# Optimization experiments

Hardware: AMD Instinct MI355X
Metric: run time of the kernel (lower is better)

The kernel has to match this reference:

```python
import jax, jax.numpy as jnp
import numpy as np

B, C, H, W = 4, 256, 64, 64
CR = max(C // 8, 1)  # reduced channels
EPS = 1e-12  # F.normalize eps


def setup_inputs() -> dict:
    key = jax.random.key(0)
    ks = jax.random.split(key, 8)
    s = 1.0 / np.sqrt(C)
    return {
        "x": jax.random.normal(ks[0], (B, C, H, W), dtype=jnp.float32),
        "Wq": jax.random.normal(ks[1], (CR, C), dtype=jnp.float32) * s,
        "bq": jax.random.normal(ks[2], (CR,), dtype=jnp.float32) * s,
        "Wk": jax.random.normal(ks[3], (CR, C), dtype=jnp.float32) * s,
        "bk": jax.random.normal(ks[4], (CR,), dtype=jnp.float32) * s,
        "Wv": jax.random.normal(ks[5], (C, C), dtype=jnp.float32) * s,
        "bv": jax.random.normal(ks[6], (C,), dtype=jnp.float32) * s,
        "gamma": jax.random.normal(ks[7], (1,), dtype=jnp.float32),
    }


def reference(x, Wq, bq, Wk, bk, Wv, bv, gamma):
    b, c, h, w = x.shape
    xf = x.reshape(b, c, h * w)  # [B, C, N]
    # 1x1 convs are per-pixel linear maps
    q = jnp.einsum("rc,bcn->brn", Wq, xf) + bq[None, :, None]  # [B, CR, N]
    k = jnp.einsum("rc,bcn->brn", Wk, xf) + bk[None, :, None]  # [B, CR, N]
    v = jnp.einsum("dc,bcn->bdn", Wv, xf) + bv[None, :, None]  # [B, C, N]
    # attention = bmm(key^T, query): [B, N, N]
    attn = jnp.einsum("brn,brm->bnm", k, q)
    attn = jax.nn.relu(attn)
    # L1 normalize along dim=1 (rows), matching F.normalize(p=1, dim=1)
    denom = jnp.maximum(jnp.sum(jnp.abs(attn), axis=1, keepdims=True), EPS)
    attn = attn / denom
    out = jnp.einsum("bcn,bnm->bcm", v, attn).reshape(b, c, h, w)
    return gamma[0] * out + x
```

## Files before the change

### kernel.cpp

```cpp
#include <hip/hip_runtime.h>
#include <hip/hip_bf16.h>

#define NB 4
#define NC 256
#define NN 4096
#define NCR 32

typedef __attribute__((ext_vector_type(8))) short short8_t;
typedef __attribute__((ext_vector_type(4))) float f32x4;
typedef __attribute__((ext_vector_type(2))) int int2_t;
typedef __attribute__((ext_vector_type(4))) int int4_t;
typedef __attribute__((ext_vector_type(4))) float float4_t;

static __device__ __forceinline__ unsigned short f2bf(float f) {
  unsigned u = __builtin_bit_cast(unsigned, f);
  u += 0x7FFFu + ((u >> 16) & 1u);
  return (unsigned short)(u >> 16);
}

static __device__ __forceinline__ unsigned cvt_pk(float lo, float hi) {
  unsigned r;
  asm("v_cvt_pk_bf16_f32 %0, %1, %2" : "=v"(r) : "v"(lo), "v"(hi));
  return r;
}

__global__ __launch_bounds__(64) void pack_w_kernel(
    const float* __restrict__ Wq, const float* __restrict__ Wk,
    const float* __restrict__ Wv, unsigned short* __restrict__ Wbf)
{
  const int row = blockIdx.x;
  const int t = threadIdx.x;
  const float* src = row < 32 ? Wq + (size_t)row * NC
                   : (row < 64 ? Wk + (size_t)(row - 32) * NC
                               : Wv + (size_t)(row - 64) * NC);
  float4_t v = *(const float4_t*)(src + t * 4);
  int2_t p;
  p[0] = cvt_pk(v[0], v[1]);
  p[1] = cvt_pk(v[2], v[3]);
  *(int2_t*)(Wbf + (size_t)row * NC + t * 4) = p;
}

__global__ __launch_bounds__(256) void qkv_kernel(
    const float* __restrict__ x, const unsigned short* __restrict__ Wbf,
    const float* __restrict__ bq, const float* __restrict__ bk,
    const float* __restrict__ bv,
    unsigned short* __restrict__ Qt, unsigned short* __restrict__ Kt,
    unsigned short* __restrict__ Vt)
{
  __shared__ unsigned short xT[2][64 * 32];

  const int bid = blockIdx.x;
  const int b   = bid >> 6;
  const int m0  = (bid & 63) * 64;
  const int tid = threadIdx.x;
  const int w    = tid >> 6;
  const int lane = tid & 63;
  const int lg   = lane >> 4;
  const int lm   = lane & 15;

  const float* xb = x + (size_t)b * NC * NN;
  const float* xld = xb + (size_t)(8 * w) * NN + m0 + lane;
  const int wofs = lane * 32 + ((w ^ (lane & 3)) << 3);
  const unsigned short* wrow = Wbf + (size_t)(w * 80 + lm) * NC;

  const f32x4 zero4 = {0.f, 0.f, 0.f, 0.f};
  f32x4 acc[5][4];
#pragma unroll
  for (int df = 0; df < 5; df++)
#pragma unroll
    for (int mf = 0; mf < 4; mf++) acc[df][mf] = zero4;

  float xg[8], xn[8];
#pragma unroll
  for (int j = 0; j < 8; j++) xg[j] = xld[j * NN];

#define QSTEP(KC, XC, XN, BUF) {                                              \
    if ((KC) < 7) {                                                           \
      _Pragma("unroll") for (int j = 0; j < 8; j++)                           \
        XN[j] = xld[(((KC) + 1) * 32 + j) * NN];                              \
    }                                                                         \
    short8_t wf[5];                                                           \
    _Pragma("unroll") for (int df = 0; df < 5; df++)                          \
      wf[df] = *(const short8_t*)(wrow + df * 16 * NC + (KC) * 32 + lg * 8);  \
    int4_t xw;                                                                \
    xw[0] = cvt_pk(XC[0], XC[1]); xw[1] = cvt_pk(XC[2], XC[3]);               \
    xw[2] = cvt_pk(XC[4], XC[5]); xw[3] = cvt_pk(XC[6], XC[7]);               \
    *(int4_t*)(&xT[BUF][wofs]) = xw;                                          \
    __syncthreads();                                                          \
    short8_t xf[4];                                                           \
    _Pragma("unroll") for (int mf = 0; mf < 4; mf++)                          \
      xf[mf] = *(const short8_t*)(&xT[BUF][(mf * 16 + lm) * 32 +              \
                                          ((lg ^ (lm & 3)) << 3)]);           \
    _Pragma("unroll") for (int df = 0; df < 5; df++)                          \
      _Pragma("unroll") for (int mf = 0; mf < 4; mf++)                        \
        acc[df][mf] = __builtin_amdgcn_mfma_f32_16x16x32_bf16(                \
            xf[mf], wf[df], acc[df][mf], 0, 0, 0);                            \
  }

#pragma unroll
  for (int kc = 0; kc < 8; kc += 2) {
    QSTEP(kc, xg, xn, 0)
    QSTEP(kc + 1, xn, xg, 1)
  }
#undef QSTEP

#pragma unroll
  for (int df = 0; df < 5; df++) {
    const int dbase = w * 80 + df * 16;
    if (dbase < 64) {
      const bool isq = dbase < 32;
      const float bia = isq ? bq[dbase + lm] : bk[dbase - 32 + lm];
      unsigned short* dst = isq ? Qt : Kt;
      const int dcol = (isq ? dbase : dbase - 32) + lm;
#pragma unroll
      for (int mf = 0; mf < 4; mf++)
#pragma unroll
        for (int i = 0; i < 4; i++) {
          const int m = m0 + mf * 16 + lg * 4 + i;
          dst[((size_t)b * NN + m) * NCR + dcol] = f2bf(acc[df][mf][i] + bia);
        }
    } else {
      const int c = dbase - 64 + lm;
      const float bia = bv[c];
#pragma unroll
      for (int mf = 0; mf < 4; mf++) {
        int2_t p;
        p[0] = cvt_pk(acc[df][mf][0] + bia, acc[df][mf][1] + bia);
        p[1] = cvt_pk(acc[df][mf][2] + bia, acc[df][mf][3] + bia);
        *(int2_t*)(Vt + ((size_t)b * NC + c) * NN + m0 + mf * 16 + lg * 4) = p;
      }
    }
  }
}

__global__ __launch_bounds__(256) void attn_kernel(
    const unsigned short* __restrict__ Qt, const unsigned short* __restrict__ Kt,
    const unsigned short* __restrict__ Vt, const float* __restrict__ x,
    const float* __restrict__ gamma, float* __restrict__ out)
{
  __shared__ unsigned short Slds[2][64 * 72];
  __shared__ float dlds[4][64];

  int bid = blockIdx.x;
  bid = (bid & 7) * 32 + (bid >> 3);
  const int b   = bid >> 6;
  const int m0  = (bid & 63) * 64;
  const int tid = threadIdx.x;
  const int w    = tid >> 6;
  const int lane = tid & 63;
  const int lg   = lane >> 4;
  const int lm   = lane & 15;

  const unsigned short* Qb = Qt + (size_t)b * NN * NCR;
  const unsigned short* Kb = Kt + (size_t)b * NN * NCR + (w * 16 + lm) * NCR + lg * 8;
  const unsigned short* Vb = Vt + (size_t)b * NC * NN;
  const unsigned short* pV[4];
#pragma unroll
  for (int cf = 0; cf < 4; cf++)
    pV[cf] = Vb + (size_t)(w * 64 + cf * 16 + lm) * NN + lg * 8;

  short8_t qf[4];
#pragma unroll
  for (int mf = 0; mf < 4; mf++)
    qf[mf] = *(const short8_t*)(Qb + (size_t)(m0 + mf * 16 + lm) * NCR + lg * 8);

  const f32x4 zero4 = {0.f, 0.f, 0.f, 0.f};
  f32x4 acc[4][4];
#pragma unroll
  for (int cf = 0; cf < 4; cf++)
#pragma unroll
    for (int mf = 0; mf < 4; mf++) acc[cf][mf] = zero4;
  float dsum[4] = {0.f, 0.f, 0.f, 0.f};

  short8_t kA, kB, vA[4][2], vB[4][2];
  kA = *(const short8_t*)(Kb);
#pragma unroll
  for (int cf = 0; cf < 4; cf++)
#pragma unroll
    for (int nch = 0; nch < 2; nch++)
      vA[cf][nch] = *(const short8_t*)(pV[cf] + nch * 32);

  const int swofs = w * 16 + lg * 4;

#define AITER(T, VC, VN, KC, KN, BUF) {                                       \
    const int n1 = (((T) + 1) & 63) * 64;                                     \
    KN = *(const short8_t*)(Kb + (size_t)n1 * NCR);                           \
    _Pragma("unroll") for (int cf = 0; cf < 4; cf++)                          \
      _Pragma("unroll") for (int nch = 0; nch < 2; nch++)                     \
        VN[cf][nch] = *(const short8_t*)(pV[cf] + n1 + nch * 32);             \
    _Pragma("unroll") for (int mf = 0; mf < 4; mf++) {                        \
      f32x4 s = __builtin_amdgcn_mfma_f32_16x16x32_bf16(KC, qf[mf], zero4, 0, 0, 0); \
      float s0 = fmaxf(s[0], 0.f), s1 = fmaxf(s[1], 0.f);                     \
      float s2 = fmaxf(s[2], 0.f), s3 = fmaxf(s[3], 0.f);                     \
      dsum[mf] += (s0 + s1) + (s2 + s3);                                      \
      int2_t p; p[0] = cvt_pk(s0, s1); p[1] = cvt_pk(s2, s3);                 \
      *(int2_t*)(&Slds[BUF][(mf * 16 + lm) * 72 + swofs]) = p;                \
    }                                                                         \
    __syncthreads();                                                          \
    _Pragma("unroll") for (int nch = 0; nch < 2; nch++) {                     \
      short8_t sf[4];                                                         \
      _Pragma("unroll") for (int mf = 0; mf < 4; mf++)                        \
        sf[mf] = *(const short8_t*)(&Slds[BUF][(mf * 16 + lm) * 72 + nch * 32 + lg * 8]); \
      _Pragma("unroll") for (int cf = 0; cf < 4; cf++)                        \
        _Pragma("unroll") for (int mf = 0; mf < 4; mf++)                      \
          acc[cf][mf] = __builtin_amdgcn_mfma_f32_16x16x32_bf16(              \
              VC[cf][nch], sf[mf], acc[cf][mf], 0, 0, 0);                     \
    }                                                                         \
  }

#pragma unroll 1
  for (int t = 0; t < 64; t += 2) {
    AITER(t, vA, vB, kA, kB, 0)
    AITER(t + 1, vB, vA, kB, kA, 1)
  }
#undef AITER

#pragma unroll
  for (int mf = 0; mf < 4; mf++) {
    float v = dsum[mf];
    v += __shfl_xor(v, 16);
    v += __shfl_xor(v, 32);
    dsum[mf] = v;
  }
  if (lane < 16) {
#pragma unroll
    for (int mf = 0; mf < 4; mf++) dlds[w][mf * 16 + lane] = dsum[mf];
  }
  __syncthreads();

  const float g0 = gamma[0];
  float rden[4];
#pragma unroll
  for (int mf = 0; mf < 4; mf++) {
    const int mloc = mf * 16 + lm;
    float den = dlds[0][mloc] + dlds[1][mloc] + dlds[2][mloc] + dlds[3][mloc];
    den = den > 1e-12f ? den : 1e-12f;
    rden[mf] = 1.0f / den;
  }

  const float* xb = x + (size_t)b * NC * NN;
  float* ob = out + (size_t)b * NC * NN;
#pragma unroll
  for (int cf = 0; cf < 4; cf++) {
#pragma unroll
    for (int i = 0; i < 4; i++) {
      const int c = w * 64 + cf * 16 + lg * 4 + i;
#pragma unroll
      for (int mf = 0; mf < 4; mf++) {
        const int m = m0 + mf * 16 + lm;
        ob[(size_t)c * NN + m] = g0 * acc[cf][mf][i] * rden[mf] + xb[(size_t)c * NN + m];
      }
    }
  }
}

extern "C" void kernel_launch(void* const* d_in, const int* in_sizes, int n_in,
                              void* d_out, int out_size, void* d_ws, size_t ws_size,
                              hipStream_t stream) {
  const float* x     = (const float*)d_in[0];
  const float* Wq    = (const float*)d_in[1];
  const float* bq    = (const float*)d_in[2];
  const float* Wk    = (const float*)d_in[3];
  const float* bk    = (const float*)d_in[4];
  const float* Wv    = (const float*)d_in[5];
  const float* bv    = (const float*)d_in[6];
  const float* gamma = (const float*)d_in[7];
  float* out = (float*)d_out;

  unsigned short* Wbf = (unsigned short*)d_ws;
  unsigned short* Qt  = Wbf + (size_t)320 * NC;
  unsigned short* Kt  = Qt + (size_t)NB * NN * NCR;
  unsigned short* Vt  = Kt + (size_t)NB * NN * NCR;

  hipLaunchKernelGGL(pack_w_kernel, dim3(320), dim3(64), 0, stream,
                     Wq, Wk, Wv, Wbf);
  hipLaunchKernelGGL(qkv_kernel, dim3(256), dim3(256), 0, stream,
                     x, Wbf, bq, bk, bv, Qt, Kt, Vt);
  hipLaunchKernelGGL(attn_kernel, dim3(256), dim3(256), 0, stream,
                     Qt, Kt, Vt, x, gamma, out);
}
```

Measured before the change: 88.24 us.

## Split attention channels across blocks and precompute bf16 transposed input

Adds a kernel that transposes x to a bf16 [B,N,C] layout, so qkv_kernel reads MFMA fragments straight from global memory with no LDS staging, using 32-pixel tiles and twice as many blocks. The attention kernel now splits the 256 output channels into two halves across blocks, giving 512 blocks with 2 waves' worth of occupancy. It also maps batch and half to XCD id, drops V double-buffering in favour of in-iteration loads, and raises wave priority around the MFMA section. The cost is recomputing the QK scores twice (once per channel half), an extra kernel launch, and a round trip for the transposed x buffer.

```diff
diff --git a/kernel.cpp b/kernel.cpp
--- a/kernel.cpp
+++ b/kernel.cpp
@@ -5,6 +5,7 @@
 #define NC 256
 #define NN 4096
 #define NCR 32
+#define PITCH 72
 
 typedef __attribute__((ext_vector_type(8))) short short8_t;
 typedef __attribute__((ext_vector_type(4))) float f32x4;
@@ -40,69 +41,69 @@
   *(int2_t*)(Wbf + (size_t)row * NC + t * 4) = p;
 }
 
-__global__ __launch_bounds__(256) void qkv_kernel(
-    const float* __restrict__ x, const unsigned short* __restrict__ Wbf,
+__global__ __launch_bounds__(256) void xpose_kernel(
+    const float* __restrict__ x, unsigned short* __restrict__ xT)
+{
+  __shared__ float tile[32][65];
+  const int bid = blockIdx.x;
+  const int mt = bid & 63, kt = (bid >> 6) & 7, b = bid >> 9;
+  const int m0 = mt * 64, k0 = kt * 32;
+  const int tid = threadIdx.x;
+
+  const float* xb = x + (size_t)b * NC * NN + (size_t)k0 * NN + m0;
+#pragma unroll
+  for (int p = 0; p < 8; p++) {
+    const int r = p * 4 + (tid >> 6);
+    tile[r][tid & 63] = xb[(size_t)r * NN + (tid & 63)];
+  }
+  __syncthreads();
+
+  const int m = tid >> 2, kq = (tid & 3) * 8;
+  int4_t o;
+#pragma unroll
+  for (int j = 0; j < 4; j++)
+    o[j] = cvt_pk(tile[kq + 2 * j][m], tile[kq + 2 * j + 1][m]);
+  *(int4_t*)(xT + ((size_t)b * NN + m0 + m) * NC + k0 + kq) = o;
+}
+
+__global__ __launch_bounds__(256, 2) void qkv_kernel(
+    const unsigned short* __restrict__ xT, const unsigned short* __restrict__ Wbf,
     const float* __restrict__ bq, const float* __restrict__ bk,
     const float* __restrict__ bv,
     unsigned short* __restrict__ Qt, unsigned short* __restrict__ Kt,
     unsigned short* __restrict__ Vt)
 {
-  __shared__ unsigned short xT[2][64 * 32];
-
   const int bid = blockIdx.x;
-  const int b   = bid >> 6;
-  const int m0  = (bid & 63) * 64;
+  const int b   = bid >> 7;
+  const int m0  = (bid & 127) * 32;
   const int tid = threadIdx.x;
   const int w    = tid >> 6;
   const int lane = tid & 63;
   const int lg   = lane >> 4;
   const int lm   = lane & 15;
 
-  const float* xb = x + (size_t)b * NC * NN;
-  const float* xld = xb + (size_t)(8 * w) * NN + m0 + lane;
-  const int wofs = lane * 32 + ((w ^ (lane & 3)) << 3);
-  const unsigned short* wrow = Wbf + (size_t)(w * 80 + lm) * NC;
+  const unsigned short* xrow0 = xT + ((size_t)b * NN + m0 + lm) * NC + lg * 8;
+  const unsigned short* xrow1 = xrow0 + 16 * NC;
+  const unsigned short* wrow  = Wbf + (size_t)(w * 80 + lm) * NC + lg * 8;
 
   const f32x4 zero4 = {0.f, 0.f, 0.f, 0.f};
-  f32x4 acc[5][4];
+  f32x4 acc[5][2];
 #pragma unroll
   for (int df = 0; df < 5; df++)
 #pragma unroll
-    for (int mf = 0; mf < 4; mf++) acc[df][mf] = zero4;
-
-  float xg[8], xn[8];
-#pragma unroll
-  for (int j = 0; j < 8; j++) xg[j] = xld[j * NN];
-
-#define QSTEP(KC, XC, XN, BUF) {                                              \
-    if ((KC) < 7) {                                                           \
-      _Pragma("unroll") for (int j = 0; j < 8; j++)                           \
-        XN[j] = xld[(((KC) + 1) * 32 + j) * NN];                              \
-    }                                                                         \
-    short8_t wf[5];                                                           \
-    _Pragma("unroll") for (int df = 0; df < 5; df++)                          \
-      wf[df] = *(const short8_t*)(wrow + df * 16 * NC + (KC) * 32 + lg * 8);  \
-    int4_t xw;                                                                \
-    xw[0] = cvt_pk(XC[0], XC[1]); xw[1] = cvt_pk(XC[2], XC[3]);               \
-    xw[2] = cvt_pk(XC[4], XC[5]); xw[3] = cvt_pk(XC[6], XC[7]);               \
-    *(int4_t*)(&xT[BUF][wofs]) = xw;                                          \
-    __syncthreads();                                                          \
-    short8_t xf[4];                                                           \
-    _Pragma("unroll") for (int mf = 0; mf < 4; mf++)                          \
-      xf[mf] = *(const short8_t*)(&xT[BUF][(mf * 16 + lm) * 32 +              \
-                                          ((lg ^ (lm & 3)) << 3)]);           \
-    _Pragma("unroll") for (int df = 0; df < 5; df++)                          \
-      _Pragma("unroll") for (int mf = 0; mf < 4; mf++)                        \
-        acc[df][mf] = __builtin_amdgcn_mfma_f32_16x16x32_bf16(                \
-            xf[mf], wf[df], acc[df][mf], 0, 0, 0);                            \
-  }
-
-#pragma unroll
-  for (int kc = 0; kc < 8; kc += 2) {
-    QSTEP(kc, xg, xn, 0)
-    QSTEP(kc + 1, xn, xg, 1)
-  }
-#undef QSTEP
+    for (int mf = 0; mf < 2; mf++) acc[df][mf] = zero4;
+
+#pragma unroll
+  for (int kc = 0; kc < 8; kc++) {
+    const short8_t xf0 = *(const short8_t*)(xrow0 + kc * 32);
+    const short8_t xf1 = *(const short8_t*)(xrow1 + kc * 32);
+#pragma unroll
+    for (int df = 0; df < 5; df++) {
+      const short8_t wf = *(const short8_t*)(wrow + (size_t)df * 16 * NC + kc * 32);
+      acc[df][0] = __builtin_amdgcn_mfma_f32_16x16x32_bf16(xf0, wf, acc[df][0], 0, 0, 0);
+      acc[df][1] = __builtin_amdgcn_mfma_f32_16x16x32_bf16(xf1, wf, acc[df][1], 0, 0, 0);
+    }
+  }
 
 #pragma unroll
   for (int df = 0; df < 5; df++) {
@@ -113,7 +114,7 @@
       unsigned short* dst = isq ? Qt : Kt;
       const int dcol = (isq ? dbase : dbase - 32) + lm;
 #pragma unroll
-      for (int mf = 0; mf < 4; mf++)
+      for (int mf = 0; mf < 2; mf++)
 #pragma unroll
         for (int i = 0; i < 4; i++) {
           const int m = m0 + mf * 16 + lg * 4 + i;
@@ -123,7 +124,7 @@
       const int c = dbase - 64 + lm;
       const float bia = bv[c];
 #pragma unroll
-      for (int mf = 0; mf < 4; mf++) {
+      for (int mf = 0; mf < 2; mf++) {
         int2_t p;
         p[0] = cvt_pk(acc[df][mf][0] + bia, acc[df][mf][1] + bia);
         p[1] = cvt_pk(acc[df][mf][2] + bia, acc[df][mf][3] + bia);
@@ -133,18 +134,19 @@
   }
 }
 
-__global__ __launch_bounds__(256) void attn_kernel(
+__global__ __launch_bounds__(256, 2) void attn_kernel(
     const unsigned short* __restrict__ Qt, const unsigned short* __restrict__ Kt,
     const unsigned short* __restrict__ Vt, const float* __restrict__ x,
     const float* __restrict__ gamma, float* __restrict__ out)
 {
-  __shared__ unsigned short Slds[2][64 * 72];
+  __shared__ unsigned short Slds[2][64 * PITCH];
   __shared__ float dlds[4][64];
 
-  int bid = blockIdx.x;
-  bid = (bid & 7) * 32 + (bid >> 3);
-  const int b   = bid >> 6;
-  const int m0  = (bid & 63) * 64;
+  const int bid = blockIdx.x;
+  const int xcd = bid & 7;
+  const int b   = xcd >> 1;
+  const int ch  = xcd & 1;
+  const int m0  = (bid >> 3) * 64;
   const int tid = threadIdx.x;
   const int w    = tid >> 6;
   const int lane = tid & 63;
@@ -152,12 +154,12 @@
   const int lm   = lane & 15;
 
   const unsigned short* Qb = Qt + (size_t)b * NN * NCR;
-  const unsigned short* Kb = Kt + (size_t)b * NN * NCR + (w * 16 + lm) * NCR + lg * 8;
-  const unsigned short* Vb = Vt + (size_t)b * NC * NN;
-  const unsigned short* pV[4];
-#pragma unroll
-  for (int cf = 0; cf < 4; cf++)
-    pV[cf] = Vb + (size_t)(w * 64 + cf * 16 + lm) * NN + lg * 8;
+  const unsigned short* Kp = Kt + (size_t)b * NN * NCR +
+                             (size_t)(w * 16 + lm) * NCR + lg * 8;
+  const unsigned short* pV[2];
+#pragma unroll
+  for (int cf = 0; cf < 2; cf++)
+    pV[cf] = Vt + ((size_t)b * NC + ch * 128 + w * 32 + cf * 16 + lm) * NN + lg * 8;
 
   short8_t qf[4];
 #pragma unroll
@@ -165,53 +167,55 @@
     qf[mf] = *(const short8_t*)(Qb + (size_t)(m0 + mf * 16 + lm) * NCR + lg * 8);
 
   const f32x4 zero4 = {0.f, 0.f, 0.f, 0.f};
-  f32x4 acc[4][4];
-#pragma unroll
-  for (int cf = 0; cf < 4; cf++)
+  f32x4 acc[2][4];
+#pragma unroll
+  for (int cf = 0; cf < 2; cf++)
 #pragma unroll
     for (int mf = 0; mf < 4; mf++) acc[cf][mf] = zero4;
   float dsum[4] = {0.f, 0.f, 0.f, 0.f};
 
-  short8_t kA, kB, vA[4][2], vB[4][2];
-  kA = *(const short8_t*)(Kb);
-#pragma unroll
-  for (int cf = 0; cf < 4; cf++)
-#pragma unroll
-    for (int nch = 0; nch < 2; nch++)
-      vA[cf][nch] = *(const short8_t*)(pV[cf] + nch * 32);
+  short8_t kA, kB;
+  kA = *(const short8_t*)(Kp);
 
   const int swofs = w * 16 + lg * 4;
 
-#define AITER(T, VC, VN, KC, KN, BUF) {                                       \
+#define AITER(T, KC, KN, BUF) {                                               \
+    const int ncur = (T) * 64;                                                \
+       \
+    short8_t vc[2][2];                                                        \
+    _Pragma("unroll") for (int cf = 0; cf < 2; cf++) {                        \
+      vc[cf][0] = *(const short8_t*)(pV[cf] + ncur);                          \
+      vc[cf][1] = *(const short8_t*)(pV[cf] + ncur + 32);                     \
+    }                                                                         \
     const int n1 = (((T) + 1) & 63) * 64;                                     \
-    KN = *(const short8_t*)(Kb + (size_t)n1 * NCR);                           \
-    _Pragma("unroll") for (int cf = 0; cf < 4; cf++)                          \
-      _Pragma("unroll") for (int nch = 0; nch < 2; nch++)                     \
-        VN[cf][nch] = *(const short8_t*)(pV[cf] + n1 + nch * 32);             \
+    KN = *(const short8_t*)(Kp + (size_t)n1 * NCR);                           \
     _Pragma("unroll") for (int mf = 0; mf < 4; mf++) {                        \
       f32x4 s = __builtin_amdgcn_mfma_f32_16x16x32_bf16(KC, qf[mf], zero4, 0, 0, 0); \
       float s0 = fmaxf(s[0], 0.f), s1 = fmaxf(s[1], 0.f);                     \
       float s2 = fmaxf(s[2], 0.f), s3 = fmaxf(s[3], 0.f);                     \
       dsum[mf] += (s0 + s1) + (s2 + s3);                                      \
       int2_t p; p[0] = cvt_pk(s0, s1); p[1] = cvt_pk(s2, s3);                 \
-      *(int2_t*)(&Slds[BUF][(mf * 16 + lm) * 72 + swofs]) = p;                \
+      *(int2_t*)(&Slds[BUF][(mf * 16 + lm) * PITCH + swofs]) = p;             \
     }                                                                         \
     __syncthreads();                                                          \
+    __builtin_amdgcn_s_setprio(1);                                            \
     _Pragma("unroll") for (int nch = 0; nch < 2; nch++) {                     \
       short8_t sf[4];                                                         \
       _Pragma("unroll") for (int mf = 0; mf < 4; mf++)                        \
-        sf[mf] = *(const short8_t*)(&Slds[BUF][(mf * 16 + lm) * 72 + nch * 32 + lg * 8]); \
-      _Pragma("unroll") for (int cf = 0; cf < 4; cf++)                        \
+        sf[mf] = *(const short8_t*)(&Slds[BUF][(mf * 16 + lm) * PITCH +       \
+                                              nch * 32 + lg * 8]);            \
+      _Pragma("unroll") for (int cf = 0; cf < 2; cf++)                        \
         _Pragma("unroll") for (int mf = 0; mf < 4; mf++)                      \
           acc[cf][mf] = __builtin_amdgcn_mfma_f32_16x16x32_bf16(              \
-              VC[cf][nch], sf[mf], acc[cf][mf], 0, 0, 0);                     \
+              vc[cf][nch], sf[mf], acc[cf][mf], 0, 0, 0);                     \
     }                                                                         \
+    __builtin_amdgcn_s_setprio(0);                                            \
   }
 
 #pragma unroll 1
   for (int t = 0; t < 64; t += 2) {
-    AITER(t, vA, vB, kA, kB, 0)
-    AITER(t + 1, vB, vA, kB, kA, 1)
+    AITER(t, kA, kB, 0)
+    AITER(t + 1, kB, kA, 1)
   }
 #undef AITER
 
@@ -220,11 +224,7 @@
     float v = dsum[mf];
     v += __shfl_xor(v, 16);
     v += __shfl_xor(v, 32);
-    dsum[mf] = v;
-  }
-  if (lane < 16) {
-#pragma unroll
-    for (int mf = 0; mf < 4; mf++) dlds[w][mf * 16 + lane] = dsum[mf];
+    if (lane < 16) dlds[w][mf * 16 + lane] = v;
   }
   __syncthreads();
 
@@ -241,10 +241,10 @@
   const float* xb = x + (size_t)b * NC * NN;
   float* ob = out + (size_t)b * NC * NN;
 #pragma unroll
-  for (int cf = 0; cf < 4; cf++) {
+  for (int cf = 0; cf < 2; cf++) {
 #pragma unroll
     for (int i = 0; i < 4; i++) {
-      const int c = w * 64 + cf * 16 + lg * 4 + i;
+      const int c = ch * 128 + w * 32 + cf * 16 + lg * 4 + i;
 #pragma unroll
       for (int mf = 0; mf < 4; mf++) {
         const int m = m0 + mf * 16 + lm;
@@ -268,14 +268,16 @@
   float* out = (float*)d_out;
 
   unsigned short* Wbf = (unsigned short*)d_ws;
-  unsigned short* Qt  = Wbf + (size_t)320 * NC;
+  unsigned short* xT  = Wbf + (size_t)320 * NC;
+  unsigned short* Qt  = xT + (size_t)NB * NN * NC;
   unsigned short* Kt  = Qt + (size_t)NB * NN * NCR;
   unsigned short* Vt  = Kt + (size_t)NB * NN * NCR;
 
   hipLaunchKernelGGL(pack_w_kernel, dim3(320), dim3(64), 0, stream,
                      Wq, Wk, Wv, Wbf);
-  hipLaunchKernelGGL(qkv_kernel, dim3(256), dim3(256), 0, stream,
-                     x, Wbf, bq, bk, bv, Qt, Kt, Vt);
-  hipLaunchKernelGGL(attn_kernel, dim3(256), dim3(256), 0, stream,
+  hipLaunchKernelGGL(xpose_kernel, dim3(2048), dim3(256), 0, stream, x, xT);
+  hipLaunchKernelGGL(qkv_kernel, dim3(512), dim3(256), 0, stream,
+                     xT, Wbf, bq, bk, bv, Qt, Kt, Vt);
+  hipLaunchKernelGGL(attn_kernel, dim3(512), dim3(256), 0, stream,
                      Qt, Kt, Vt, x, gamma, out);
 }
```

Result: slower. 102.3 us (+16.0%).
